# Performance work log

Hardware: AMD Instinct MI355X
Metric: run time of the kernel (lower is better)

## Reference

```python
import jax, jax.numpy as jnp
import numpy as np

B, HH, WW, C = 8, 128, 128, 128
NH = 4          # total heads; each branch uses NH//2
SS = 2          # split_size
EPS = 1e-5


def setup_inputs() -> dict:
    key = jax.random.key(0)
    ks = jax.random.split(key, 10)
    Ch = C // 2
    Dff = 4 * C
    return {
        "x": jax.random.normal(ks[0], (B, HH * WW, C), jnp.float32),
        "ln1_g": jnp.ones((C,), jnp.float32),
        "ln1_b": jnp.zeros((C,), jnp.float32),
        "w_qkv": jax.random.normal(ks[1], (3 * C, C), jnp.float32) * 0.02,
        "w_proj": jax.random.normal(ks[2], (C, C), jnp.float32) * 0.02,
        "b_proj": jnp.zeros((C,), jnp.float32),
        "conv_w0": jax.random.normal(ks[3], (Ch, 1, 3, 3), jnp.float32) * 0.02,
        "conv_b0": jnp.zeros((Ch,), jnp.float32),
        "conv_w1": jax.random.normal(ks[4], (Ch, 1, 3, 3), jnp.float32) * 0.02,
        "conv_b1": jnp.zeros((Ch,), jnp.float32),
        "ln2_g": jnp.ones((C,), jnp.float32),
        "ln2_b": jnp.zeros((C,), jnp.float32),
        "w1": jax.random.normal(ks[5], (Dff, C), jnp.float32) * 0.02,
        "b1": jnp.zeros((Dff,), jnp.float32),
        "w2": jax.random.normal(ks[6], (C, Dff), jnp.float32) * 0.02,
        "b2": jnp.zeros((C,), jnp.float32),
        "H": HH,
        "W": WW,
    }


def _layernorm(x, g, b):
    m = jnp.mean(x, axis=-1, keepdims=True)
    v = jnp.mean(jnp.square(x - m), axis=-1, keepdims=True)
    return (x - m) * jax.lax.rsqrt(v + EPS) * g + b


def _cswin_branch(q, k, v, conv_w, conv_b, H, W, H_sp, W_sp, heads):
    """q,k,v: [B, H*W, Ch] -> [B, H*W, Ch] cross-shaped-window LePE attention."""
    Bq, L, Ch = q.shape
    hd = Ch // heads
    T = H_sp * W_sp
    nh, nw = H // H_sp, W // W_sp

    def to_win(t):  # [B,L,Ch] -> [nW*B, heads, T, hd]
        t = t.reshape(Bq, nh, H_sp, nw, W_sp, Ch).transpose(0, 1, 3, 2, 4, 5)
        return t.reshape(-1, T, heads, hd).transpose(0, 2, 1, 3)

    qw, kw = to_win(q), to_win(k)

    # v as window images [nW*B, Ch, H_sp, W_sp] for depthwise LePE conv
    vimg = v.reshape(Bq, nh, H_sp, nw, W_sp, Ch).transpose(0, 1, 3, 5, 2, 4)
    vimg = vimg.reshape(-1, Ch, H_sp, W_sp)
    lepe = jax.lax.conv_general_dilated(
        vimg, conv_w, window_strides=(1, 1), padding="SAME",
        feature_group_count=Ch,
        dimension_numbers=("NCHW", "OIHW", "NCHW"),
    ) + conv_b[None, :, None, None]
    lepe = lepe.reshape(-1, heads, hd, T).transpose(0, 1, 3, 2)  # [nW*B,h,T,hd]
    vw = vimg.reshape(-1, heads, hd, T).transpose(0, 1, 3, 2)

    scale = hd ** -0.5
    attn = jnp.einsum("whtd,whsd->whts", qw * scale, kw)
    attn = jax.nn.softmax(attn, axis=-1)
    out = jnp.einsum("whts,whsd->whtd", attn, vw) + lepe  # [nW*B,h,T,hd]

    out = out.transpose(0, 2, 1, 3).reshape(-1, T, Ch)
    out = out.reshape(Bq, nh, nw, H_sp, W_sp, Ch).transpose(0, 1, 3, 2, 4, 5)
    return out.reshape(Bq, H * W, Ch)


def reference(x, ln1_g, ln1_b, w_qkv, w_proj, b_proj, conv_w0, conv_b0,
              conv_w1, conv_b1, ln2_g, ln2_b, w1, b1, w2, b2, H, W):
    Bx, L, Cx = x.shape
    Ch = Cx // 2
    heads = NH // 2

    img = _layernorm(x, ln1_g, ln1_b)
    qkv = (img @ w_qkv.T).reshape(Bx, L, 3, Cx)
    q, k, v = qkv[:, :, 0, :], qkv[:, :, 1, :], qkv[:, :, 2, :]

    # idx=0: horizontal stripes (H_sp=H, W_sp=SS); idx=1: vertical (H_sp=SS, W_sp=W)
    x1 = _cswin_branch(q[..., :Ch], k[..., :Ch], v[..., :Ch],
                       conv_w0, conv_b0, H, W, H, SS, heads)
    x2 = _cswin_branch(q[..., Ch:], k[..., Ch:], v[..., Ch:],
                       conv_w1, conv_b1, H, W, SS, W, heads)
    att = jnp.concatenate([x1, x2], axis=2)
    att = att @ w_proj.T + b_proj

    x = x + att
    h = _layernorm(x, ln2_g, ln2_b)
    h = jax.nn.gelu(h @ w1.T + b1, approximate=False) @ w2.T + b2
    return x + h
```

## Files before the change

kernel.cpp:

```cpp
#include <hip/hip_runtime.h>
#include <cstddef>


#define LDIM 16384
#define NTOK 131072
#define PLANE ((size_t)NTOK * 128)

typedef __attribute__((ext_vector_type(8))) short bf16x8;
typedef __attribute__((ext_vector_type(4))) float f32x4;

__device__ __forceinline__ unsigned short f2bf(float f) {
  union { float f; unsigned int i; } u; u.f = f;
  unsigned int r = u.i + 0x7fffu + ((u.i >> 16) & 1u);
  return (unsigned short)(r >> 16);
}
__device__ __forceinline__ float bflo(unsigned int u) {
  union { unsigned int i; float f; } x; x.i = u << 16; return x.f;
}
__device__ __forceinline__ unsigned int pk(float a, float b) {
  return (unsigned)f2bf(a) | ((unsigned)f2bf(b) << 16);
}

__device__ __forceinline__ void async16(const unsigned short* g, unsigned short* l) {
  __builtin_amdgcn_global_load_lds(
      (const __attribute__((address_space(1))) unsigned int*)g,
      (__attribute__((address_space(3))) unsigned int*)l, 16, 0, 0);
}

__device__ __forceinline__ void barrier_lgkm() {
  asm volatile("s_waitcnt lgkmcnt(0)" ::: "memory");
  __builtin_amdgcn_s_barrier();
  __builtin_amdgcn_sched_barrier(0);
}

__device__ __forceinline__ bf16x8 fragS(const unsigned short* base, int row, int c) {
  return *(const bf16x8*)(base + row * 128 + ((c ^ (row & 7)) << 3));
}

__device__ __forceinline__ bf16x8 ldw(const unsigned short* p) {
  return *(const bf16x8*)p;
}

__device__ __forceinline__ void stageS128(const unsigned short* __restrict__ src, int rowStride,
                                          unsigned short* dst, int tid) {
  const int lane = tid & 63, wv = tid >> 6;
  #pragma unroll
  for (int i = 0; i < 8; i++) {
    const int base = i * 256 + wv * 64;
    const int f = base + lane;
    const int row = f >> 4, cs = f & 15, cg = cs ^ (row & 7);
    async16(src + (size_t)row * rowStride + (cg << 3), dst + (size_t)base * 8);
  }
}

__device__ __forceinline__ void stageS64(const unsigned short* __restrict__ src,
                                         unsigned short* dst, int tid) {
  const int lane = tid & 63, wv = tid >> 6;
  #pragma unroll
  for (int i = 0; i < 4; i++) {
    const int base = i * 256 + wv * 64;
    const int f = base + lane;
    const int row = f >> 4, cs = f & 15, cg = cs ^ (row & 7);
    async16(src + (size_t)row * 128 + (cg << 3), dst + (size_t)base * 8);
  }
}

__device__ __forceinline__ void gemmS(const unsigned short* As, const unsigned short* Bs,
                                      f32x4 acc[4][4], int wm, int wn, int q, int r) {
  #pragma unroll
  for (int kc = 0; kc < 4; kc++) {
    bf16x8 a[4], b[4];
    #pragma unroll
    for (int mt = 0; mt < 4; mt++) a[mt] = fragS(As, wm * 64 + mt * 16 + r, kc * 4 + q);
    #pragma unroll
    for (int nt = 0; nt < 4; nt++) b[nt] = fragS(Bs, wn * 64 + nt * 16 + r, kc * 4 + q);
    #pragma unroll
    for (int mt = 0; mt < 4; mt++)
      #pragma unroll
      for (int nt = 0; nt < 4; nt++)
        acc[mt][nt] = __builtin_amdgcn_mfma_f32_16x16x32_bf16(a[mt], b[nt], acc[mt][nt], 0, 0, 0);
  }
}

__device__ __forceinline__ void storeC(f32x4 acc[4][4], unsigned short* Cs,
                                       unsigned short* __restrict__ dst, int dstStride, int tid) {
  const int wv = tid >> 6, lane = tid & 63, q = lane >> 4, r = lane & 15;
  const int wm = wv & 1, wn = wv >> 1;
  #pragma unroll
  for (int mt = 0; mt < 4; mt++)
    #pragma unroll
    for (int nt = 0; nt < 4; nt++) {
      const int col = wn * 64 + nt * 16 + r;
      #pragma unroll
      for (int rg = 0; rg < 4; rg++) {
        const int row = wm * 64 + mt * 16 + q * 4 + rg;
        Cs[row * 128 + ((((col >> 3) ^ (row & 7)) << 3) | (col & 7))] = f2bf(acc[mt][nt][rg]);
      }
    }
  __syncthreads();
  #pragma unroll
  for (int i = 0; i < 8; i++) {
    const int f = tid + i * 256;
    const int row = f >> 4, cs = f & 15, cg = cs ^ (row & 7);
    *(uint4*)(dst + (size_t)row * dstStride + (cg << 3)) = *(const uint4*)(Cs + row * 128 + cs * 8);
  }
}

__device__ __forceinline__ float gelu_t(float x) {
  const float y = -2.3022083f * (x + 0.044715f * x * x * x);
  const float p = __builtin_amdgcn_exp2f(y);
  return x * __builtin_amdgcn_rcpf(1.f + p);
}

__global__ void k_prep(const float* __restrict__ wq, const float* __restrict__ wp,
                       const float* __restrict__ w1, const float* __restrict__ w2,
                       unsigned short* __restrict__ wb)
{
  const int id = blockIdx.x * 256 + threadIdx.x;
  const float* src; int off;
  if (id < 12288)      { src = wq; off = id; }
  else if (id < 16384) { src = wp; off = id - 12288; }
  else if (id < 32768) { src = w1; off = id - 16384; }
  else                 { src = w2; off = id - 32768; }
  const float4 v = *(const float4*)(src + (size_t)off * 4);
  uint2 u; u.x = pk(v.x, v.y); u.y = pk(v.z, v.w);
  *(uint2*)(wb + (size_t)id * 4) = u;
}

__global__ __launch_bounds__(256, 2) void k_ln_qkv(
    const float* __restrict__ x, const float* __restrict__ g, const float* __restrict__ bb,
    const unsigned short* __restrict__ wqkvb, unsigned short* __restrict__ qkv)
{
  __shared__ unsigned short xs[128 * 128];
  __shared__ unsigned short ws[128 * 128];
  __shared__ float redS[128][2], redQ[128][2];
  const int tid = threadIdx.x;
  const long m0 = (long)blockIdx.x * 128;

  stageS128(wqkvb, 128, ws, tid);

  {
    const int m = tid >> 1, hf = tid & 1;
    const float4* xg = (const float4*)(x + (size_t)(m0 + m) * 128 + hf * 64);
    float4 xv[16];
    #pragma unroll
    for (int i = 0; i < 16; i++) xv[i] = xg[i];
    float s1 = 0.f, s2 = 0.f;
    #pragma unroll
    for (int i = 0; i < 16; i++) {
      s1 += xv[i].x + xv[i].y + xv[i].z + xv[i].w;
      s2 += xv[i].x * xv[i].x + xv[i].y * xv[i].y + xv[i].z * xv[i].z + xv[i].w * xv[i].w;
    }
    redS[m][hf] = s1; redQ[m][hf] = s2;
    __syncthreads();
    const float mean = (redS[m][0] + redS[m][1]) * (1.f / 128.f);
    const float var  = (redQ[m][0] + redQ[m][1]) * (1.f / 128.f) - mean * mean;
    const float rs = rsqrtf(var + 1e-5f);
    const float4* g4 = (const float4*)(g + hf * 64);
    const float4* b4 = (const float4*)(bb + hf * 64);
    #pragma unroll
    for (int i = 0; i < 8; i++) {
      float4 v0 = xv[2 * i], v1 = xv[2 * i + 1];
      float4 g0 = g4[2 * i], g1 = g4[2 * i + 1], p0 = b4[2 * i], p1 = b4[2 * i + 1];
      uint4 u;
      u.x = pk((v0.x - mean) * rs * g0.x + p0.x, (v0.y - mean) * rs * g0.y + p0.y);
      u.y = pk((v0.z - mean) * rs * g0.z + p0.z, (v0.w - mean) * rs * g0.w + p0.w);
      u.z = pk((v1.x - mean) * rs * g1.x + p1.x, (v1.y - mean) * rs * g1.y + p1.y);
      u.w = pk((v1.z - mean) * rs * g1.z + p1.z, (v1.w - mean) * rs * g1.w + p1.w);
      const int c = hf * 8 + i;
      *(uint4*)&xs[m * 128 + ((c ^ (m & 7)) << 3)] = u;
    }
  }
  const int lane = tid & 63, q = lane >> 4, r = lane & 15;
  const int wv = tid >> 6, wm = wv & 1, wn = wv >> 1;
  for (int nc = 0; nc < 3; nc++) {
    __syncthreads();
    if (nc > 0) {
      stageS128(wqkvb + (size_t)nc * 16384, 128, ws, tid);
      __syncthreads();
    }
    f32x4 acc[4][4];
    #pragma unroll
    for (int a = 0; a < 4; a++)
      #pragma unroll
      for (int b = 0; b < 4; b++) acc[a][b] = f32x4{0.f, 0.f, 0.f, 0.f};
    gemmS(xs, ws, acc, wm, wn, q, r);
    __syncthreads();
    storeC(acc, ws, qkv + (size_t)nc * PLANE + (size_t)m0 * 128, 128, tid);
  }
}

__global__ __launch_bounds__(256, 2) void k_attn(
    const unsigned short* __restrict__ qkv,
    const float* __restrict__ conv_w0, const float* __restrict__ conv_b0,
    const float* __restrict__ conv_w1, const float* __restrict__ conv_b1,
    unsigned short* __restrict__ att)
{
  __shared__ unsigned short Kt[256][40];
  __shared__ unsigned short Vt[32][264];
  __shared__ unsigned short Ps[4][64][72];
  const unsigned short* kpl = qkv + PLANE;
  const unsigned short* vpl = qkv + 2 * PLANE;
  const int t = threadIdx.x;
  const int win = blockIdx.x, head = blockIdx.y, br = blockIdx.z;
  const int bimg = win >> 6, widx = win & 63;
  const int c0 = br * 64 + head * 32;
  const int lgWs = (br == 0) ? 1 : 7;
  const int Wsm1 = (1 << lgWs) - 1;
  const long base = (long)bimg * LDIM + ((br == 0) ? widx * 2 : widx * 256);

  {
    const long tj = base + (long)(t >> lgWs) * 128 + (t & Wsm1);
    const uint4* kp = (const uint4*)(kpl + (size_t)tj * 128 + c0);
    uint4 k0v = kp[0], k1v = kp[1], k2v = kp[2], k3v = kp[3];
    *(uint4*)&Kt[t][0]  = k0v;  *(uint4*)&Kt[t][8]  = k1v;
    *(uint4*)&Kt[t][16] = k2v;  *(uint4*)&Kt[t][24] = k3v;
    const uint4* vp = (const uint4*)(vpl + (size_t)tj * 128 + c0);
    uint4 vv[4] = {vp[0], vp[1], vp[2], vp[3]};
    const unsigned short* vs = (const unsigned short*)vv;
    #pragma unroll
    for (int d = 0; d < 32; d++) Vt[d][t] = vs[d];
  }
  const int wave = t >> 6, lane = t & 63, q = lane >> 4, r = lane & 15;
  const int qbase = wave * 64;
  bf16x8 qf[4];
  #pragma unroll
  for (int mt = 0; mt < 4; mt++) {
    const int row = qbase + mt * 16 + r;
    const long tok = base + (long)(row >> lgWs) * 128 + (row & Wsm1);
    qf[mt] = *(const bf16x8*)(qkv + (size_t)tok * 128 + c0 + q * 8);
  }
  __syncthreads();

  const float factor = 0.17677669529663687f * 1.44269504088896341f;
  f32x4 Oacc[4][2];
  float psum[4][4];
  #pragma unroll
  for (int mt = 0; mt < 4; mt++) {
    Oacc[mt][0] = f32x4{0.f, 0.f, 0.f, 0.f};
    Oacc[mt][1] = f32x4{0.f, 0.f, 0.f, 0.f};
    #pragma unroll
    for (int rg = 0; rg < 4; rg++) psum[mt][rg] = 0.f;
  }

  for (int kc = 0; kc < 4; kc++) {
    bf16x8 kb[4];
    #pragma unroll
    for (int nt = 0; nt < 4; nt++) kb[nt] = *(const bf16x8*)&Kt[kc * 64 + nt * 16 + r][q * 8];
    f32x4 s[4][4];
    #pragma unroll
    for (int mt = 0; mt < 4; mt++)
      #pragma unroll
      for (int nt = 0; nt < 4; nt++) {
        f32x4 z = f32x4{0.f, 0.f, 0.f, 0.f};
        s[mt][nt] = __builtin_amdgcn_mfma_f32_16x16x32_bf16(qf[mt], kb[nt], z, 0, 0, 0);
      }
    #pragma unroll
    for (int mt = 0; mt < 4; mt++)
      #pragma unroll
      for (int nt = 0; nt < 4; nt++)
        #pragma unroll
        for (int rg = 0; rg < 4; rg++) {
          const float p = __builtin_amdgcn_exp2f(s[mt][nt][rg] * factor);
          psum[mt][rg] += p;
          Ps[wave][mt * 16 + q * 4 + rg][nt * 16 + r] = f2bf(p);
        }
    #pragma unroll
    for (int kst = 0; kst < 2; kst++) {
      bf16x8 pa[4], vb[2];
      #pragma unroll
      for (int mt = 0; mt < 4; mt++) pa[mt] = *(const bf16x8*)&Ps[wave][mt * 16 + r][kst * 32 + q * 8];
      #pragma unroll
      for (int nto = 0; nto < 2; nto++) vb[nto] = *(const bf16x8*)&Vt[nto * 16 + r][kc * 64 + kst * 32 + q * 8];
      #pragma unroll
      for (int mt = 0; mt < 4; mt++)
        #pragma unroll
        for (int nto = 0; nto < 2; nto++)
          Oacc[mt][nto] = __builtin_amdgcn_mfma_f32_16x16x32_bf16(pa[mt], vb[nto], Oacc[mt][nto], 0, 0, 0);
    }
  }

  #pragma unroll
  for (int mt = 0; mt < 4; mt++)
    #pragma unroll
    for (int rg = 0; rg < 4; rg++) {
      float v = psum[mt][rg];
      v += __shfl_xor(v, 1); v += __shfl_xor(v, 2);
      v += __shfl_xor(v, 4); v += __shfl_xor(v, 8);
      psum[mt][rg] = __builtin_amdgcn_rcpf(v);
    }

  const float* cw = br ? conv_w1 : conv_w0;
  const float* cb = br ? conv_b1 : conv_b0;
  float wle[2][9], ble[2];
  #pragma unroll
  for (int nto = 0; nto < 2; nto++) {
    const int ch = head * 32 + nto * 16 + r;
    ble[nto] = cb[ch];
    #pragma unroll
    for (int tp = 0; tp < 9; tp++) wle[nto][tp] = cw[ch * 9 + tp];
  }
  const int WsW = 1 << lgWs;
  const int HsW = 256 >> lgWs;

  #pragma unroll
  for (int mt = 0; mt < 4; mt++)
    #pragma unroll
    for (int rg = 0; rg < 4; rg++) {
      const int row = qbase + mt * 16 + q * 4 + rg;
      const int ii = row >> lgWs, jj = row & Wsm1;
      const long tok = base + (long)ii * 128 + jj;
      float lep0 = ble[0], lep1 = ble[1];
      #pragma unroll
      for (int di = -1; di <= 1; di++) {
        if ((unsigned)(ii + di) >= (unsigned)HsW) continue;
        #pragma unroll
        for (int dj = -1; dj <= 1; dj++) {
          if ((unsigned)(jj + dj) >= (unsigned)WsW) continue;
          const int nb = row + di * WsW + dj;
          const int tap = (di + 1) * 3 + (dj + 1);
          lep0 = fmaf(bflo(Vt[r][nb]),      wle[0][tap], lep0);
          lep1 = fmaf(bflo(Vt[16 + r][nb]), wle[1][tap], lep1);
        }
      }
      const float pr = psum[mt][rg];
      att[(size_t)tok * 128 + c0 + r]      = f2bf(Oacc[mt][0][rg] * pr + lep0);
      att[(size_t)tok * 128 + c0 + 16 + r] = f2bf(Oacc[mt][1][rg] * pr + lep1);
    }
}

__global__ __launch_bounds__(256, 2) void k_projmlp(
    const unsigned short* __restrict__ att, const unsigned short* __restrict__ wprojb,
    const float* __restrict__ b_proj, const float* __restrict__ x,
    const float* __restrict__ g, const float* __restrict__ bb,
    const unsigned short* __restrict__ w1b, const unsigned short* __restrict__ w2b,
    const float* __restrict__ b1, const float* __restrict__ b2,
    float* __restrict__ out)
{
  __shared__ unsigned short hs[64 * 128];
  __shared__ unsigned short xs[64 * 128 + 16384];
  __shared__ float redS[64][4], redQ[64][4];
  const int tid = threadIdx.x;
  const long m0 = (long)blockIdx.x * 64;
  const int lane = tid & 63, q = lane >> 4, r = lane & 15, wv = tid >> 6;

  stageS64(att + (size_t)m0 * 128, hs, tid);

  bf16x8 wcur[8];
  #pragma unroll
  for (int kc = 0; kc < 4; kc++)
    #pragma unroll
    for (int nt = 0; nt < 2; nt++)
      wcur[kc * 2 + nt] = ldw(wprojb + (size_t)(wv * 32 + nt * 16 + r) * 128 + kc * 32 + q * 8);

  float xv[4][2][4];
  #pragma unroll
  for (int mt = 0; mt < 4; mt++)
    #pragma unroll
    for (int nt = 0; nt < 2; nt++) {
      const int col = wv * 32 + nt * 16 + r;
      #pragma unroll
      for (int rg = 0; rg < 4; rg++)
        xv[mt][nt][rg] = x[(size_t)(m0 + mt * 16 + q * 4 + rg) * 128 + col];
    }
  float bpv[2], gv[2], bv2[2], b1v[4][2], b2v[2];
  #pragma unroll
  for (int nt = 0; nt < 2; nt++) {
    const int col = wv * 32 + nt * 16 + r;
    bpv[nt] = b_proj[col]; gv[nt] = g[col]; bv2[nt] = bb[col]; b2v[nt] = b2[col];
    #pragma unroll
    for (int nc = 0; nc < 4; nc++) b1v[nc][nt] = b1[nc * 128 + col];
  }
  __syncthreads();

  f32x4 xres[4][2];
  #pragma unroll
  for (int mt = 0; mt < 4; mt++) { xres[mt][0] = f32x4{0.f,0.f,0.f,0.f}; xres[mt][1] = f32x4{0.f,0.f,0.f,0.f}; }
  #pragma unroll
  for (int kc = 0; kc < 4; kc++) {
    bf16x8 a[4];
    #pragma unroll
    for (int mt = 0; mt < 4; mt++) a[mt] = fragS(hs, mt * 16 + r, kc * 4 + q);
    #pragma unroll
    for (int mt = 0; mt < 4; mt++)
      #pragma unroll
      for (int nt = 0; nt < 2; nt++)
        xres[mt][nt] = __builtin_amdgcn_mfma_f32_16x16x32_bf16(a[mt], wcur[kc * 2 + nt], xres[mt][nt], 0, 0, 0);
  }
  bf16x8 wnxt[8];
  #pragma unroll
  for (int kc = 0; kc < 4; kc++)
    #pragma unroll
    for (int nt = 0; nt < 2; nt++)
      wnxt[kc * 2 + nt] = ldw(w1b + (size_t)(wv * 32 + nt * 16 + r) * 128 + kc * 32 + q * 8);

  #pragma unroll
  for (int mt = 0; mt < 4; mt++)
    #pragma unroll
    for (int nt = 0; nt < 2; nt++)
      #pragma unroll
      for (int rg = 0; rg < 4; rg++)
        xres[mt][nt][rg] += xv[mt][nt][rg] + bpv[nt];

  #pragma unroll
  for (int mt = 0; mt < 4; mt++)
    #pragma unroll
    for (int rg = 0; rg < 4; rg++) {
      float s1 = xres[mt][0][rg] + xres[mt][1][rg];
      float s2 = xres[mt][0][rg] * xres[mt][0][rg] + xres[mt][1][rg] * xres[mt][1][rg];
      s1 += __shfl_xor(s1, 1); s1 += __shfl_xor(s1, 2); s1 += __shfl_xor(s1, 4); s1 += __shfl_xor(s1, 8);
      s2 += __shfl_xor(s2, 1); s2 += __shfl_xor(s2, 2); s2 += __shfl_xor(s2, 4); s2 += __shfl_xor(s2, 8);
      if (r == 0) { const int row = mt * 16 + q * 4 + rg; redS[row][wv] = s1; redQ[row][wv] = s2; }
    }
  barrier_lgkm();
  #pragma unroll
  for (int mt = 0; mt < 4; mt++)
    #pragma unroll
    for (int rg = 0; rg < 4; rg++) {
      const int row = mt * 16 + q * 4 + rg;
      const float s1 = redS[row][0] + redS[row][1] + redS[row][2] + redS[row][3];
      const float s2 = redQ[row][0] + redQ[row][1] + redQ[row][2] + redQ[row][3];
      const float mean = s1 * (1.f / 128.f);
      const float var  = s2 * (1.f / 128.f) - mean * mean;
      const float rs = rsqrtf(var + 1e-5f);
      #pragma unroll
      for (int nt = 0; nt < 2; nt++) {
        const int col = wv * 32 + nt * 16 + r;
        const float v = (xres[mt][nt][rg] - mean) * rs * gv[nt] + bv2[nt];
        xs[row * 128 + ((((col >> 3) ^ (row & 7)) << 3) | (col & 7))] = f2bf(v);
      }
    }
  barrier_lgkm();

  f32x4 oacc[4][2];
  #pragma unroll
  for (int mt = 0; mt < 4; mt++) { oacc[mt][0] = f32x4{0.f,0.f,0.f,0.f}; oacc[mt][1] = f32x4{0.f,0.f,0.f,0.f}; }

  for (int nc = 0; nc < 4; nc++) {
    #pragma unroll
    for (int i = 0; i < 8; i++) wcur[i] = wnxt[i];
    #pragma unroll
    for (int kc = 0; kc < 4; kc++)
      #pragma unroll
      for (int nt = 0; nt < 2; nt++)
        wnxt[kc * 2 + nt] = ldw(w2b + (size_t)(wv * 32 + nt * 16 + r) * 512 + nc * 128 + kc * 32 + q * 8);
    f32x4 h[4][2];
    #pragma unroll
    for (int mt = 0; mt < 4; mt++) { h[mt][0] = f32x4{0.f,0.f,0.f,0.f}; h[mt][1] = f32x4{0.f,0.f,0.f,0.f}; }
    #pragma unroll
    for (int kc = 0; kc < 4; kc++) {
      bf16x8 a[4];
      #pragma unroll
      for (int mt = 0; mt < 4; mt++) a[mt] = fragS(xs, mt * 16 + r, kc * 4 + q);
      #pragma unroll
      for (int mt = 0; mt < 4; mt++)
        #pragma unroll
        for (int nt = 0; nt < 2; nt++)
          h[mt][nt] = __builtin_amdgcn_mfma_f32_16x16x32_bf16(a[mt], wcur[kc * 2 + nt], h[mt][nt], 0, 0, 0);
    }
    barrier_lgkm();
    #pragma unroll
    for (int mt = 0; mt < 4; mt++)
      #pragma unroll
      for (int nt = 0; nt < 2; nt++) {
        const int col = wv * 32 + nt * 16 + r;
        const float bv = b1v[nc][nt];
        #pragma unroll
        for (int rg = 0; rg < 4; rg++) {
          const int rw = mt * 16 + q * 4 + rg;
          hs[rw * 128 + ((((col >> 3) ^ (rw & 7)) << 3) | (col & 7))] = f2bf(gelu_t(h[mt][nt][rg] + bv));
        }
      }
    barrier_lgkm();
    #pragma unroll
    for (int i = 0; i < 8; i++) wcur[i] = wnxt[i];
    if (nc < 3) {
      #pragma unroll
      for (int kc = 0; kc < 4; kc++)
        #pragma unroll
        for (int nt = 0; nt < 2; nt++)
          wnxt[kc * 2 + nt] = ldw(w1b + (size_t)((nc + 1) * 128 + wv * 32 + nt * 16 + r) * 128 + kc * 32 + q * 8);
    }
    #pragma unroll
    for (int kc = 0; kc < 4; kc++) {
      bf16x8 a[4];
      #pragma unroll
      for (int mt = 0; mt < 4; mt++) a[mt] = fragS(hs, mt * 16 + r, kc * 4 + q);
      #pragma unroll
      for (int mt = 0; mt < 4; mt++)
        #pragma unroll
        for (int nt = 0; nt < 2; nt++)
          oacc[mt][nt] = __builtin_amdgcn_mfma_f32_16x16x32_bf16(a[mt], wcur[kc * 2 + nt], oacc[mt][nt], 0, 0, 0);
    }
  }
  #pragma unroll
  for (int mt = 0; mt < 4; mt++)
    #pragma unroll
    for (int nt = 0; nt < 2; nt++) {
      const float bv = b2v[nt];
      const int col = wv * 32 + nt * 16 + r;
      #pragma unroll
      for (int rg = 0; rg < 4; rg++) {
        const size_t idx = (size_t)(m0 + mt * 16 + q * 4 + rg) * 128 + col;
        out[idx] = xres[mt][nt][rg] + bv + oacc[mt][nt][rg];
      }
    }
}

extern "C" void kernel_launch(void* const* d_in, const int* in_sizes, int n_in,
                              void* d_out, int out_size, void* d_ws, size_t ws_size,
                              hipStream_t stream) {
  const float* x       = (const float*)d_in[0];
  const float* ln1_g   = (const float*)d_in[1];
  const float* ln1_b   = (const float*)d_in[2];
  const float* w_qkv   = (const float*)d_in[3];
  const float* w_proj  = (const float*)d_in[4];
  const float* b_proj  = (const float*)d_in[5];
  const float* conv_w0 = (const float*)d_in[6];
  const float* conv_b0 = (const float*)d_in[7];
  const float* conv_w1 = (const float*)d_in[8];
  const float* conv_b1 = (const float*)d_in[9];
  const float* ln2_g   = (const float*)d_in[10];
  const float* ln2_b   = (const float*)d_in[11];
  const float* w1      = (const float*)d_in[12];
  const float* b1      = (const float*)d_in[13];
  const float* w2      = (const float*)d_in[14];
  const float* b2      = (const float*)d_in[15];
  float* out = (float*)d_out;

  unsigned short* qkv = (unsigned short*)d_ws;
  unsigned short* att = qkv;
  unsigned short* wb  = qkv + 3 * PLANE;
  unsigned short* wqkvb  = wb;
  unsigned short* wprojb = wb + 49152;
  unsigned short* w1b    = wb + 65536;
  unsigned short* w2b    = wb + 131072;

  k_prep<<<dim3(192), 256, 0, stream>>>(w_qkv, w_proj, w1, w2, wb);
  k_ln_qkv<<<dim3(NTOK / 128), 256, 0, stream>>>(x, ln1_g, ln1_b, wqkvb, qkv);
  k_attn<<<dim3(512, 2, 2), 256, 0, stream>>>(qkv, conv_w0, conv_b0, conv_w1, conv_b1, att);
  k_projmlp<<<dim3(NTOK / 64), 256, 0, stream>>>(att, wprojb, b_proj, x, ln2_g, ln2_b,
                                                 w1b, w2b, b1, b2, out);
}
```

Before: 348.0 us.

## Keep softmax probabilities in registers via transposed QK^T and lane shuffles

The attention kernel now computes S^T by swapping the MFMA operands, so each lane holds one query column's scores. The exponentials are packed to bf16 with a hardware cvt instruction and redistributed with cross-lane shuffles into the A-operand layout for the PV MFMA, which removes the per-wave Ps shared-memory staging buffer. Row sums are reduced across lane groups and applied to the output accumulators before the LePE add. Dropping the LDS buffer lets launch bounds rise to three blocks per CU. The cost is many extra shuffles and selects per tile, plus higher register pressure under the tighter occupancy bound.

```diff
diff --git a/kernel.cpp b/kernel.cpp
--- a/kernel.cpp
+++ b/kernel.cpp
@@ -19,6 +19,11 @@
 }
 __device__ __forceinline__ unsigned int pk(float a, float b) {
   return (unsigned)f2bf(a) | ((unsigned)f2bf(b) << 16);
+}
+__device__ __forceinline__ unsigned int cvtpk(float a, float b) {
+  unsigned int r;
+  asm("v_cvt_pk_bf16_f32 %0, %1, %2" : "=v"(r) : "v"(a), "v"(b));
+  return r;
 }
 
 __device__ __forceinline__ void async16(const unsigned short* g, unsigned short* l) {
@@ -190,7 +195,7 @@
   }
 }
 
-__global__ __launch_bounds__(256, 2) void k_attn(
+__global__ __launch_bounds__(256, 3) void k_attn(
     const unsigned short* __restrict__ qkv,
     const float* __restrict__ conv_w0, const float* __restrict__ conv_b0,
     const float* __restrict__ conv_w1, const float* __restrict__ conv_b1,
@@ -198,7 +203,6 @@
 {
   __shared__ unsigned short Kt[256][40];
   __shared__ unsigned short Vt[32][264];
-  __shared__ unsigned short Ps[4][64][72];
   const unsigned short* kpl = qkv + PLANE;
   const unsigned short* vpl = qkv + 2 * PLANE;
   const int t = threadIdx.x;
@@ -234,61 +238,79 @@
 
   const float factor = 0.17677669529663687f * 1.44269504088896341f;
   f32x4 Oacc[4][2];
-  float psum[4][4];
+  float part[4];
   #pragma unroll
   for (int mt = 0; mt < 4; mt++) {
     Oacc[mt][0] = f32x4{0.f, 0.f, 0.f, 0.f};
     Oacc[mt][1] = f32x4{0.f, 0.f, 0.f, 0.f};
-    #pragma unroll
-    for (int rg = 0; rg < 4; rg++) psum[mt][rg] = 0.f;
-  }
+    part[mt] = 0.f;
+  }
+  const int la = ((lane >> 4) & 1) * 32 + r;
+  const int lb = la + 16;
+  const bool hiq = (lane & 32) != 0;
 
   for (int kc = 0; kc < 4; kc++) {
-    bf16x8 kb[4];
-    #pragma unroll
-    for (int nt = 0; nt < 4; nt++) kb[nt] = *(const bf16x8*)&Kt[kc * 64 + nt * 16 + r][q * 8];
-    f32x4 s[4][4];
-    #pragma unroll
-    for (int mt = 0; mt < 4; mt++)
-      #pragma unroll
-      for (int nt = 0; nt < 4; nt++) {
+    unsigned int pk32[4][4][2];
+    #pragma unroll
+    for (int nt = 0; nt < 4; nt++) {
+      const bf16x8 kb = *(const bf16x8*)&Kt[kc * 64 + nt * 16 + r][q * 8];
+      f32x4 s4[4];
+      #pragma unroll
+      for (int mt = 0; mt < 4; mt++) {
         f32x4 z = f32x4{0.f, 0.f, 0.f, 0.f};
-        s[mt][nt] = __builtin_amdgcn_mfma_f32_16x16x32_bf16(qf[mt], kb[nt], z, 0, 0, 0);
-      }
-    #pragma unroll
-    for (int mt = 0; mt < 4; mt++)
-      #pragma unroll
-      for (int nt = 0; nt < 4; nt++)
-        #pragma unroll
-        for (int rg = 0; rg < 4; rg++) {
-          const float p = __builtin_amdgcn_exp2f(s[mt][nt][rg] * factor);
-          psum[mt][rg] += p;
-          Ps[wave][mt * 16 + q * 4 + rg][nt * 16 + r] = f2bf(p);
-        }
+        s4[mt] = __builtin_amdgcn_mfma_f32_16x16x32_bf16(kb, qf[mt], z, 0, 0, 0);
+      }
+      #pragma unroll
+      for (int mt = 0; mt < 4; mt++) {
+        const float p0 = __builtin_amdgcn_exp2f(s4[mt][0] * factor);
+        const float p1 = __builtin_amdgcn_exp2f(s4[mt][1] * factor);
+        const float p2 = __builtin_amdgcn_exp2f(s4[mt][2] * factor);
+        const float p3 = __builtin_amdgcn_exp2f(s4[mt][3] * factor);
+        part[mt] += (p0 + p1) + (p2 + p3);
+        pk32[nt][mt][0] = cvtpk(p0, p1);
+        pk32[nt][mt][1] = cvtpk(p2, p3);
+      }
+    }
     #pragma unroll
     for (int kst = 0; kst < 2; kst++) {
-      bf16x8 pa[4], vb[2];
-      #pragma unroll
-      for (int mt = 0; mt < 4; mt++) pa[mt] = *(const bf16x8*)&Ps[wave][mt * 16 + r][kst * 32 + q * 8];
-      #pragma unroll
-      for (int nto = 0; nto < 2; nto++) vb[nto] = *(const bf16x8*)&Vt[nto * 16 + r][kc * 64 + kst * 32 + q * 8];
-      #pragma unroll
-      for (int mt = 0; mt < 4; mt++)
+      bf16x8 vb[2];
+      #pragma unroll
+      for (int nto = 0; nto < 2; nto++)
+        vb[nto] = *(const bf16x8*)&Vt[nto * 16 + r][kc * 64 + kst * 32 + q * 8];
+      #pragma unroll
+      for (int mt = 0; mt < 4; mt++) {
+        const unsigned int a0 = __shfl(pk32[kst * 2][mt][0], la);
+        const unsigned int a1 = __shfl(pk32[kst * 2][mt][1], la);
+        const unsigned int a2 = __shfl(pk32[kst * 2][mt][0], lb);
+        const unsigned int a3 = __shfl(pk32[kst * 2][mt][1], lb);
+        const unsigned int b0 = __shfl(pk32[kst * 2 + 1][mt][0], la);
+        const unsigned int b1 = __shfl(pk32[kst * 2 + 1][mt][1], la);
+        const unsigned int b2 = __shfl(pk32[kst * 2 + 1][mt][0], lb);
+        const unsigned int b3 = __shfl(pk32[kst * 2 + 1][mt][1], lb);
+        union { uint4 u; bf16x8 v; } cv;
+        cv.u.x = hiq ? b0 : a0;
+        cv.u.y = hiq ? b1 : a1;
+        cv.u.z = hiq ? b2 : a2;
+        cv.u.w = hiq ? b3 : a3;
         #pragma unroll
         for (int nto = 0; nto < 2; nto++)
-          Oacc[mt][nto] = __builtin_amdgcn_mfma_f32_16x16x32_bf16(pa[mt], vb[nto], Oacc[mt][nto], 0, 0, 0);
-    }
-  }
-
-  #pragma unroll
-  for (int mt = 0; mt < 4; mt++)
+          Oacc[mt][nto] = __builtin_amdgcn_mfma_f32_16x16x32_bf16(cv.v, vb[nto], Oacc[mt][nto], 0, 0, 0);
+      }
+    }
+  }
+
+  #pragma unroll
+  for (int mt = 0; mt < 4; mt++) {
+    float v = part[mt];
+    v += __shfl_xor(v, 16); v += __shfl_xor(v, 32);
+    v = __builtin_amdgcn_rcpf(v);
     #pragma unroll
     for (int rg = 0; rg < 4; rg++) {
-      float v = psum[mt][rg];
-      v += __shfl_xor(v, 1); v += __shfl_xor(v, 2);
-      v += __shfl_xor(v, 4); v += __shfl_xor(v, 8);
-      psum[mt][rg] = __builtin_amdgcn_rcpf(v);
-    }
+      const float s = __shfl(v, (lane & 48) + q * 4 + rg);
+      Oacc[mt][0][rg] *= s;
+      Oacc[mt][1][rg] *= s;
+    }
+  }
 
   const float* cw = br ? conv_w1 : conv_w0;
   const float* cb = br ? conv_b1 : conv_b0;
@@ -323,9 +345,8 @@
           lep1 = fmaf(bflo(Vt[16 + r][nb]), wle[1][tap], lep1);
         }
       }
-      const float pr = psum[mt][rg];
-      att[(size_t)tok * 128 + c0 + r]      = f2bf(Oacc[mt][0][rg] * pr + lep0);
-      att[(size_t)tok * 128 + c0 + 16 + r] = f2bf(Oacc[mt][1][rg] * pr + lep1);
+      att[(size_t)tok * 128 + c0 + r]      = f2bf(Oacc[mt][0][rg] + lep0);
+      att[(size_t)tok * 128 + c0 + 16 + r] = f2bf(Oacc[mt][1][rg] + lep1);
     }
 }
 
```

New measurement: 325.7 us. -6.4%, faster.
